# Kernel optimization log

Hardware: AMD Instinct MI355X
Metric: run time of the kernel (lower is better)

The kernel has to match this reference:

```python
import jax, jax.numpy as jnp
import numpy as np

H = 1024      # hidden_dim
F = 4 * H     # expert FFN dim
E = 16        # num_experts
K = 4         # num_experts_per_token


def setup_inputs() -> dict:
    key = jax.random.key(0)
    ks = jax.random.split(key, 10)
    s = 0.02
    return {
        "x": jax.random.normal(ks[0], (2, 1024, H), dtype=jnp.float32),
        # router: Linear(H,H) -> ReLU -> Linear(H,E)
        "Wr1": jax.random.normal(ks[1], (H, H), dtype=jnp.float32) * s,
        "br1": jnp.zeros((H,), dtype=jnp.float32),
        "Wr2": jax.random.normal(ks[2], (H, E), dtype=jnp.float32) * s,
        "br2": jnp.zeros((E,), dtype=jnp.float32),
        # stacked experts: Linear(H,4H) -> GELU -> Linear(4H,H)
        "W1": jax.random.normal(ks[3], (E, H, F), dtype=jnp.float32) * s,
        "b1": jnp.zeros((E, F), dtype=jnp.float32),
        "W2": jax.random.normal(ks[4], (E, F, H), dtype=jnp.float32) * s,
        "b2": jnp.zeros((E, H), dtype=jnp.float32),
    }


def reference(x, Wr1, br1, Wr2, br2, W1, b1, W2, b2):
    B, S, Hd = x.shape
    xf = x.reshape(-1, Hd)                       # [T, H]
    T = xf.shape[0]
    # router logits
    logits = jnp.maximum(xf @ Wr1 + br1, 0.0) @ Wr2 + br2   # [T, E]
    # top-k routing: softmax over the k selected logits
    topw, topi = jax.lax.top_k(logits, K)                    # [T, K]
    topw = jax.nn.softmax(topw, axis=-1)
    # dense combine weights c[t, e] = sum_k topw[t,k] * 1[topi[t,k]==e]
    c = jnp.zeros((T, E), dtype=xf.dtype)
    c = c.at[jnp.arange(T)[:, None], topi].add(topw)         # [T, E]
    # all-experts dense MLP (exact GELU, matching nn.GELU default)
    h = jax.nn.gelu(jnp.einsum('th,ehf->etf', xf, W1) + b1[:, None, :],
                    approximate=False)                       # [E, T, F]
    y = jnp.einsum('etf,efh->eth', h, W2) + b2[:, None, :]   # [E, T, H]
    out = jnp.einsum('eth,te->th', y, c)                     # [T, H]
    return out.reshape(B, S, Hd)
```

## Files before the change

### kernel.cpp

```cpp
#include <hip/hip_runtime.h>
#include <hip/hip_bf16.h>

#define T_TOK 2048
#define H_DIM 1024
#define F_DIM 4096
#define E_NUM 16
#define K_TOP 4

typedef float    floatx4 __attribute__((ext_vector_type(4)));
typedef _Float16 f16x8   __attribute__((ext_vector_type(8)));
typedef _Float16 f16x4   __attribute__((ext_vector_type(4)));

#define MiB (1024ull * 1024ull)
#define LOGIT_OFF ((size_t)0)
#define TOPI_OFF  (128ull * 1024)
#define TOPW_OFF  (192ull * 1024)
#define CNT_OFF   (256ull * 1024)
#define OFFS_OFF  (CNT_OFF + 256)
#define CUR_OFF   (OFFS_OFF + 256)
#define TOKS_OFF  (320ull * 1024)
#define WSL_OFF   (384ull * 1024)
#define STK_OFF   (448ull * 1024)
#define TILEE_OFF (512ull * 1024)
#define TILEM_OFF (TILEE_OFF + 512)
#define TILEC_OFF (TILEM_OFF + 512)
#define XH_OFF    (1ull * MiB)
#define HBUF_OFF  (8ull * MiB)
#define YBUF_OFF  (72ull * MiB)
#define W1T_OFF   (104ull * MiB)
#define W2T_OFF   (232ull * MiB)
#define WS_NEED_FAST (360ull * MiB)

__device__ __forceinline__ void gload16(const void* g, void* l) {
  __builtin_amdgcn_global_load_lds(
      (const __attribute__((address_space(1))) unsigned int*)g,
      (__attribute__((address_space(3))) unsigned int*)l, 16, 0, 0);
}

__device__ __forceinline__ float gelu_fast(float v) {
  float z = 0.7978845608028654f * (v + 0.044715f * v * v * v);
  float e = __expf(2.f * z);
  float t = 1.f - 2.f / (e + 1.f);
  return 0.5f * v * (1.f + t);
}

__global__ void zero_counts_kernel(int* counts) {
  if (threadIdx.x < E_NUM) counts[threadIdx.x] = 0;
}

__device__ __forceinline__ void cast_x_body(int blk, const float* __restrict__ x,
                                            _Float16* __restrict__ xh) {
  int i = blk * 256 + threadIdx.x;
  const floatx4* xin = reinterpret_cast<const floatx4*>(x) + (size_t)i * 2;
  floatx4 a = xin[0], b = xin[1];
  f16x8 o;
  o[0] = (_Float16)a[0]; o[1] = (_Float16)a[1]; o[2] = (_Float16)a[2]; o[3] = (_Float16)a[3];
  o[4] = (_Float16)b[0]; o[5] = (_Float16)b[1]; o[6] = (_Float16)b[2]; o[7] = (_Float16)b[3];
  *reinterpret_cast<f16x8*>(xh + (size_t)i * 8) = o;
}

__device__ __forceinline__ void tcast_body(const float* __restrict__ W,
                                           _Float16* __restrict__ Wt, int K, int N,
                                           int e, int k0, int n0, char* smem) {
  float (*Tt)[68] = (float(*)[68])smem;
  const float* We = W + (size_t)e * K * N;
  int t = threadIdx.x;
  int kk = t >> 4, nn = (t & 15) * 4;
#pragma unroll
  for (int j = 0; j < 4; j++) {
    int k = kk + 16 * j;
    floatx4 v = *reinterpret_cast<const floatx4*>(We + (size_t)(k0 + k) * N + n0 + nn);
    *reinterpret_cast<floatx4*>(&Tt[k][nn]) = v;
  }
  __syncthreads();
  int nr = t >> 2, kc = t & 3;
  f16x8 o0, o1;
#pragma unroll
  for (int j = 0; j < 8; j++) {
    o0[j] = (_Float16)Tt[kc * 16 + j][nr];
    o1[j] = (_Float16)Tt[kc * 16 + 8 + j][nr];
  }
  _Float16* dst = Wt + (size_t)e * N * K + (size_t)(n0 + nr) * K + k0 + kc * 16;
  *reinterpret_cast<f16x8*>(dst) = o0;
  *reinterpret_cast<f16x8*>(dst + 8) = o1;
}

__device__ __forceinline__ void router_gemm1_body(
    int m0, int n0, const float* __restrict__ x, const float* __restrict__ Wr1,
    const float* __restrict__ br1, float* __restrict__ hrf, char* smem) {
  _Float16 (*Ah)[40] = (_Float16(*)[40])(smem);
  _Float16 (*Al)[40] = (_Float16(*)[40])(smem + 5120);
  _Float16 (*Bh)[40] = (_Float16(*)[40])(smem + 10240);
  _Float16 (*Bl)[40] = (_Float16(*)[40])(smem + 15360);
  int tid = threadIdx.x;
  int arow = tid >> 2, achk = tid & 3;
  const float* Arow = x + (size_t)(m0 + arow) * H_DIM + achk * 8;
  int brow = tid >> 3, bq = tid & 7;

  floatx4 acc[2][2];
#pragma unroll
  for (int i = 0; i < 2; i++)
#pragma unroll
    for (int j = 0; j < 2; j++) acc[i][j] = (floatx4){0.f, 0.f, 0.f, 0.f};

  int wv = tid >> 6, lane = tid & 63;
  int wm = wv >> 1, wn = wv & 1;
  int lrow = lane & 15, lk = (lane >> 4) * 8;

  for (int k0 = 0; k0 < H_DIM; k0 += 32) {
    floatx4 a0 = *reinterpret_cast<const floatx4*>(Arow + k0);
    floatx4 a1 = *reinterpret_cast<const floatx4*>(Arow + k0 + 4);
    f16x8 hv, lv;
#pragma unroll
    for (int j = 0; j < 4; j++) {
      _Float16 hi = (_Float16)a0[j]; hv[j] = hi; lv[j] = (_Float16)(a0[j] - (float)hi);
      _Float16 hi2 = (_Float16)a1[j]; hv[4 + j] = hi2; lv[4 + j] = (_Float16)(a1[j] - (float)hi2);
    }
    *reinterpret_cast<f16x8*>(&Ah[arow][achk * 8]) = hv;
    *reinterpret_cast<f16x8*>(&Al[arow][achk * 8]) = lv;
    const float* wp = Wr1 + (size_t)(k0 + brow) * H_DIM + n0 + bq * 4;
    floatx4 w0 = *reinterpret_cast<const floatx4*>(wp);
    floatx4 w1 = *reinterpret_cast<const floatx4*>(wp + 32);
#pragma unroll
    for (int i = 0; i < 4; i++) {
      _Float16 h0 = (_Float16)w0[i];
      Bh[bq * 4 + i][brow] = h0; Bl[bq * 4 + i][brow] = (_Float16)(w0[i] - (float)h0);
      _Float16 h1 = (_Float16)w1[i];
      Bh[32 + bq * 4 + i][brow] = h1; Bl[32 + bq * 4 + i][brow] = (_Float16)(w1[i] - (float)h1);
    }
    __syncthreads();

    f16x8 ah0 = *reinterpret_cast<const f16x8*>(&Ah[32 * wm + lrow][lk]);
    f16x8 ah1 = *reinterpret_cast<const f16x8*>(&Ah[32 * wm + 16 + lrow][lk]);
    f16x8 al0 = *reinterpret_cast<const f16x8*>(&Al[32 * wm + lrow][lk]);
    f16x8 al1 = *reinterpret_cast<const f16x8*>(&Al[32 * wm + 16 + lrow][lk]);
    f16x8 bh0 = *reinterpret_cast<const f16x8*>(&Bh[32 * wn + lrow][lk]);
    f16x8 bh1 = *reinterpret_cast<const f16x8*>(&Bh[32 * wn + 16 + lrow][lk]);
    f16x8 bl0 = *reinterpret_cast<const f16x8*>(&Bl[32 * wn + lrow][lk]);
    f16x8 bl1 = *reinterpret_cast<const f16x8*>(&Bl[32 * wn + 16 + lrow][lk]);

    acc[0][0] = __builtin_amdgcn_mfma_f32_16x16x32_f16(ah0, bh0, acc[0][0], 0, 0, 0);
    acc[0][0] = __builtin_amdgcn_mfma_f32_16x16x32_f16(ah0, bl0, acc[0][0], 0, 0, 0);
    acc[0][0] = __builtin_amdgcn_mfma_f32_16x16x32_f16(al0, bh0, acc[0][0], 0, 0, 0);
    acc[0][1] = __builtin_amdgcn_mfma_f32_16x16x32_f16(ah0, bh1, acc[0][1], 0, 0, 0);
    acc[0][1] = __builtin_amdgcn_mfma_f32_16x16x32_f16(ah0, bl1, acc[0][1], 0, 0, 0);
    acc[0][1] = __builtin_amdgcn_mfma_f32_16x16x32_f16(al0, bh1, acc[0][1], 0, 0, 0);
    acc[1][0] = __builtin_amdgcn_mfma_f32_16x16x32_f16(ah1, bh0, acc[1][0], 0, 0, 0);
    acc[1][0] = __builtin_amdgcn_mfma_f32_16x16x32_f16(ah1, bl0, acc[1][0], 0, 0, 0);
    acc[1][0] = __builtin_amdgcn_mfma_f32_16x16x32_f16(al1, bh0, acc[1][0], 0, 0, 0);
    acc[1][1] = __builtin_amdgcn_mfma_f32_16x16x32_f16(ah1, bh1, acc[1][1], 0, 0, 0);
    acc[1][1] = __builtin_amdgcn_mfma_f32_16x16x32_f16(ah1, bl1, acc[1][1], 0, 0, 0);
    acc[1][1] = __builtin_amdgcn_mfma_f32_16x16x32_f16(al1, bh1, acc[1][1], 0, 0, 0);
    __syncthreads();
  }

#pragma unroll
  for (int am = 0; am < 2; am++) {
#pragma unroll
    for (int bn = 0; bn < 2; bn++) {
      int col = n0 + 32 * wn + 16 * bn + lrow;
      float bv = br1[col];
#pragma unroll
      for (int r = 0; r < 4; r++) {
        int rowt = 32 * wm + 16 * am + (lane >> 4) * 4 + r;
        float v = acc[am][bn][r] + bv;
        hrf[(size_t)(m0 + rowt) * H_DIM + col] = fmaxf(v, 0.f);
      }
    }
  }
}

#define FA_RG   512
#define FA_TC   16384
#define FA_CX   1024
__global__ __launch_bounds__(256) void fusedA_kernel(
    const float* __restrict__ x, const float* __restrict__ Wr1, const float* __restrict__ br1,
    float* __restrict__ hrf, const float* __restrict__ W1, _Float16* __restrict__ W1t,
    _Float16* __restrict__ xh) {
  __shared__ __align__(16) char smem[20480];
  int bid = blockIdx.x;
  if (bid < FA_RG) {
    router_gemm1_body((bid >> 4) * 64, (bid & 15) * 64, x, Wr1, br1, hrf, smem);
  } else if (bid < FA_RG + FA_TC) {
    int idx = bid - FA_RG;
    int nt = idx & 63, kt = (idx >> 6) & 15, e = idx >> 10;
    tcast_body(W1, W1t, H_DIM, F_DIM, e, kt * 64, nt * 64, smem);
  } else {
    cast_x_body(bid - FA_RG - FA_TC, x, xh);
  }
}

__global__ __launch_bounds__(256) void router_logits_kernel(
    const float* __restrict__ hrf, const float* __restrict__ Wr2,
    const float* __restrict__ br2, float* __restrict__ logits) {
  int t = blockIdx.x * 4 + (threadIdx.x >> 6);
  int lane = threadIdx.x & 63;
  float acc[E_NUM];
#pragma unroll
  for (int e = 0; e < E_NUM; e++) acc[e] = 0.f;
  const float* hr = hrf + (size_t)t * H_DIM;
#pragma unroll 4
  for (int i = 0; i < H_DIM / 64; i++) {
    int k = lane + 64 * i;
    float a = hr[k];
    const floatx4* w4 = reinterpret_cast<const floatx4*>(Wr2 + (size_t)k * E_NUM);
    floatx4 w0 = w4[0], w1 = w4[1], w2 = w4[2], w3 = w4[3];
#pragma unroll
    for (int j = 0; j < 4; j++) {
      acc[j]      += a * w0[j];
      acc[4 + j]  += a * w1[j];
      acc[8 + j]  += a * w2[j];
      acc[12 + j] += a * w3[j];
    }
  }
#pragma unroll
  for (int e = 0; e < E_NUM; e++) {
    float v = acc[e];
    for (int off = 32; off > 0; off >>= 1) v += __shfl_xor(v, off);
    if (lane == e) logits[(size_t)t * E_NUM + e] = v + br2[e];
  }
}

__global__ void route_kernel(const float* __restrict__ logits, int* __restrict__ topi,
                             float* __restrict__ topw, int* __restrict__ counts) {
  int t = blockIdx.x * 256 + threadIdx.x;
  if (t >= T_TOK) return;
  float lg[E_NUM];
#pragma unroll
  for (int e = 0; e < E_NUM; e++) lg[e] = logits[(size_t)t * E_NUM + e];
  unsigned int used = 0;
  float vals[K_TOP]; int idx[K_TOP];
#pragma unroll
  for (int k = 0; k < K_TOP; k++) {
    float best = -1e30f; int bi = 0;
#pragma unroll
    for (int e = 0; e < E_NUM; e++) {
      if (!((used >> e) & 1u) && lg[e] > best) { best = lg[e]; bi = e; }
    }
    used |= (1u << bi);
    vals[k] = best; idx[k] = bi;
  }
  float m = vals[0];
  float s = 0.f;
  float w[K_TOP];
#pragma unroll
  for (int k = 0; k < K_TOP; k++) { w[k] = expf(vals[k] - m); s += w[k]; }
  float inv = 1.f / s;
#pragma unroll
  for (int k = 0; k < K_TOP; k++) {
    topi[t * K_TOP + k] = idx[k];
    topw[t * K_TOP + k] = w[k] * inv;
    atomicAdd(&counts[idx[k]], 1);
  }
}

__global__ void scan_kernel(const int* __restrict__ counts, int* __restrict__ offsets,
                            int* __restrict__ cursor, int* __restrict__ tileE,
                            int* __restrict__ tileM, int* __restrict__ tileC) {
  if (threadIdx.x == 0) {
    int acc = 0;
    offsets[0] = 0;
    for (int e = 0; e < E_NUM; e++) { acc += counts[e]; offsets[e + 1] = acc; }
    int idx = 0;
    for (int e = 0; e < E_NUM; e++) {
      int c = counts[e];
      for (int m0 = 0; m0 < c; m0 += 128) { tileE[idx] = e; tileM[idx] = m0; idx++; }
    }
    tileC[0] = idx;
  }
  if (threadIdx.x < E_NUM) cursor[threadIdx.x] = 0;
}

__global__ void scatter_kernel(const int* __restrict__ topi, const float* __restrict__ topw,
                               const int* __restrict__ offsets, int* __restrict__ cursor,
                               int* __restrict__ tok_of_slot, float* __restrict__ w_of_slot,
                               int* __restrict__ slot_of_tk) {
  int t = blockIdx.x * 256 + threadIdx.x;
  if (t >= T_TOK) return;
#pragma unroll
  for (int k = 0; k < K_TOP; k++) {
    int e = topi[t * K_TOP + k];
    int pos = atomicAdd(&cursor[e], 1);
    int slot = offsets[e] + pos;
    tok_of_slot[slot] = t;
    w_of_slot[slot] = topw[t * K_TOP + k];
    slot_of_tk[t * K_TOP + k] = slot;
  }
}

__global__ void combine_kernel(const float* __restrict__ ybuf, const int* __restrict__ slot_of_tk,
                               float* __restrict__ out) {
  int i = blockIdx.x * 256 + threadIdx.x;
  size_t p = (size_t)i * 4;
  int t = (int)(p >> 10);
  int h = (int)(p & 1023);
  float s0 = 0.f, s1 = 0.f, s2 = 0.f, s3 = 0.f;
#pragma unroll
  for (int k = 0; k < K_TOP; k++) {
    int slot = slot_of_tk[t * K_TOP + k];
    const floatx4 v = *reinterpret_cast<const floatx4*>(ybuf + (size_t)slot * H_DIM + h);
    s0 += v[0]; s1 += v[1]; s2 += v[2]; s3 += v[3];
  }
  floatx4 o = {s0, s1, s2, s3};
  *reinterpret_cast<floatx4*>(out + p) = o;
}

template <int ACT, bool GATHER, bool SCALE, bool OUTF16>
__device__ __forceinline__ void moe_gemm_body(
    int ti, int n0, const _Float16* __restrict__ A, const _Float16* __restrict__ Bt,
    const float* __restrict__ bias, void* __restrict__ Out,
    const int* __restrict__ offsets, const int* __restrict__ toklist,
    const float* __restrict__ wslot, const int* __restrict__ tileE,
    const int* __restrict__ tileM, const int* __restrict__ tileC,
    int N, int K, char* smem) {
  if (ti >= tileC[0]) return;
  int e = tileE[ti], m0 = tileM[ti];
  int base = offsets[e], cnt = offsets[e + 1] - base;

  _Float16 (*As)[128][32] = (_Float16(*)[128][32])(smem);
  _Float16 (*Bs)[128][32] = (_Float16(*)[128][32])(smem + 16384);

  int tid = threadIdx.x;
  int w = tid >> 6, lane = tid & 63;
  int wm = w >> 1, wn = w & 1;
  int lrow = lane & 15, lkc = (lane >> 4) * 8;

  int ar0 = w * 32 + (lane >> 2);
  int ar1 = ar0 + 16;
  int ach = (lane & 3) * 8;
  int mr0 = m0 + ar0; if (mr0 >= cnt) mr0 = cnt - 1;
  int mr1 = m0 + ar1; if (mr1 >= cnt) mr1 = cnt - 1;
  const _Float16* gA0 = A + (long)(GATHER ? toklist[base + mr0] : (base + mr0)) * K + ach;
  const _Float16* gA1 = A + (long)(GATHER ? toklist[base + mr1] : (base + mr1)) * K + ach;
  const _Float16* bge = Bt + (size_t)e * N * K;
  const _Float16* gB0 = bge + (long)(n0 + ar0) * K + ach;
  const _Float16* gB1 = bge + (long)(n0 + ar1) * K + ach;

#define STAGE2(buf, kk) do { \
    gload16(gA0 + (kk), &As[buf][w * 32][0]); \
    gload16(gA1 + (kk), &As[buf][w * 32 + 16][0]); \
    gload16(gB0 + (kk), &Bs[buf][w * 32][0]); \
    gload16(gB1 + (kk), &Bs[buf][w * 32 + 16][0]); \
  } while (0)

  floatx4 acc[4][4];
#pragma unroll
  for (int i = 0; i < 4; i++)
#pragma unroll
    for (int j = 0; j < 4; j++) acc[i][j] = (floatx4){0.f, 0.f, 0.f, 0.f};

  STAGE2(0, 0);
  __syncthreads();

  int nk = K >> 5;
  for (int it = 0; it < nk; ++it) {
    int cur = it & 1;
    if (it + 1 < nk) STAGE2(cur ^ 1, (it + 1) << 5);

    f16x8 a[4], b[4];
#pragma unroll
    for (int i = 0; i < 4; i++) {
      a[i] = *reinterpret_cast<const f16x8*>(&As[cur][wm * 64 + i * 16 + lrow][lkc]);
      b[i] = *reinterpret_cast<const f16x8*>(&Bs[cur][wn * 64 + i * 16 + lrow][lkc]);
    }
#pragma unroll
    for (int i = 0; i < 4; i++)
#pragma unroll
      for (int j = 0; j < 4; j++)
        acc[i][j] = __builtin_amdgcn_mfma_f32_16x16x32_f16(a[i], b[j], acc[i][j], 0, 0, 0);

    __syncthreads();
  }
#undef STAGE2

  const float* be = bias + (size_t)e * N;
#pragma unroll
  for (int fm = 0; fm < 4; fm++) {
#pragma unroll
    for (int fn = 0; fn < 4; fn++) {
      int col = n0 + wn * 64 + fn * 16 + lrow;
      float bv = be[col];
#pragma unroll
      for (int r = 0; r < 4; r++) {
        int rowt = wm * 64 + fm * 16 + (lane >> 4) * 4 + r;
        int mg = m0 + rowt;
        if (mg < cnt) {
          float v = acc[fm][fn][r] + bv;
          if (ACT == 2) v = gelu_fast(v);
          long orow = base + mg;
          if (SCALE) v *= wslot[orow];
          if (OUTF16)
            ((_Float16*)Out)[orow * (long)N + col] = (_Float16)v;
          else
            ((float*)Out)[orow * (long)N + col] = v;
        }
      }
    }
  }
}

#define FB_G1 (32 * 80)
#define FB_TC 16384
__global__ __launch_bounds__(256) void fusedB_kernel(
    const _Float16* __restrict__ xh, const _Float16* __restrict__ W1t,
    const float* __restrict__ b1, _Float16* __restrict__ hbuf,
    const int* __restrict__ offsets, const int* __restrict__ toklist,
    const int* __restrict__ tileE, const int* __restrict__ tileM, const int* __restrict__ tileC,
    const float* __restrict__ W2, _Float16* __restrict__ W2t) {
  __shared__ __align__(16) char smem[32768];
  int bid = blockIdx.x;
  if (bid < FB_G1) {
    moe_gemm_body<2, true, false, true>(bid >> 5, (bid & 31) * 128, xh, W1t, b1, (void*)hbuf,
                                        offsets, toklist, nullptr, tileE, tileM, tileC,
                                        F_DIM, H_DIM, smem);
  } else {
    int idx = bid - FB_G1;
    int nt = idx & 15, kt = (idx >> 4) & 63, e = idx >> 10;
    tcast_body(W2, W2t, F_DIM, H_DIM, e, kt * 64, nt * 64, smem);
  }
}

__global__ __launch_bounds__(256) void moe_gemm2_kernel(
    const _Float16* __restrict__ hbuf, const _Float16* __restrict__ W2t,
    const float* __restrict__ b2, float* __restrict__ ybuf,
    const int* __restrict__ offsets, const float* __restrict__ wslot,
    const int* __restrict__ tileE, const int* __restrict__ tileM, const int* __restrict__ tileC) {
  __shared__ __align__(16) char smem[32768];
  moe_gemm_body<0, false, true, false>(blockIdx.y, blockIdx.x * 128, hbuf, W2t, b2, (void*)ybuf,
                                       offsets, nullptr, wslot, tileE, tileM, tileC,
                                       H_DIM, F_DIM, smem);
}

template <int ACT, bool GATHER, bool OFFS, bool SCALE, bool OUTF16>
__global__ __launch_bounds__(256) void moe_gemm(
    const _Float16* __restrict__ A, const float* __restrict__ W,
    const float* __restrict__ bias, void* __restrict__ Out,
    const int* __restrict__ offsets, const int* __restrict__ toklist,
    const float* __restrict__ wslot, int M, int N, int K) {
  int e = blockIdx.z;
  int base = 0, cnt = M;
  if (OFFS) { base = offsets[e]; cnt = offsets[e + 1] - base; }
  int m0 = blockIdx.y * 64;
  if (m0 >= cnt) return;
  int n0 = blockIdx.x * 64;
  const float* We = W + (size_t)e * K * N;
  const float* be = bias + (size_t)e * N;

  __shared__ _Float16 As[64][40];
  __shared__ _Float16 Bs[64][40];

  int tid = threadIdx.x;
  int arow = tid >> 2, achk = tid & 3;
  int am_idx = m0 + arow; if (am_idx > cnt - 1) am_idx = cnt - 1;
  long arowg = GATHER ? (long)toklist[base + am_idx] : (long)(base + am_idx);
  const _Float16* Arow = A + arowg * (long)K + achk * 8;

  int brow = tid >> 3, bq = tid & 7;

  floatx4 acc[2][2];
#pragma unroll
  for (int i = 0; i < 2; i++)
#pragma unroll
    for (int j = 0; j < 2; j++) acc[i][j] = (floatx4){0.f, 0.f, 0.f, 0.f};

  int wv = tid >> 6, lane = tid & 63;
  int wm = wv >> 1, wn = wv & 1;
  int lrow = lane & 15, lk = (lane >> 4) * 8;

  for (int k0 = 0; k0 < K; k0 += 32) {
    *reinterpret_cast<f16x8*>(&As[arow][achk * 8]) = *reinterpret_cast<const f16x8*>(Arow + k0);
    const float* wp = We + (size_t)(k0 + brow) * N + n0 + bq * 4;
    floatx4 w0 = *reinterpret_cast<const floatx4*>(wp);
    floatx4 w1 = *reinterpret_cast<const floatx4*>(wp + 32);
#pragma unroll
    for (int i = 0; i < 4; i++) {
      Bs[bq * 4 + i][brow]      = (_Float16)w0[i];
      Bs[32 + bq * 4 + i][brow] = (_Float16)w1[i];
    }
    __syncthreads();

    f16x8 a0 = *reinterpret_cast<const f16x8*>(&As[32 * wm + lrow][lk]);
    f16x8 a1 = *reinterpret_cast<const f16x8*>(&As[32 * wm + 16 + lrow][lk]);
    f16x8 b0 = *reinterpret_cast<const f16x8*>(&Bs[32 * wn + lrow][lk]);
    f16x8 b1 = *reinterpret_cast<const f16x8*>(&Bs[32 * wn + 16 + lrow][lk]);
    acc[0][0] = __builtin_amdgcn_mfma_f32_16x16x32_f16(a0, b0, acc[0][0], 0, 0, 0);
    acc[0][1] = __builtin_amdgcn_mfma_f32_16x16x32_f16(a0, b1, acc[0][1], 0, 0, 0);
    acc[1][0] = __builtin_amdgcn_mfma_f32_16x16x32_f16(a1, b0, acc[1][0], 0, 0, 0);
    acc[1][1] = __builtin_amdgcn_mfma_f32_16x16x32_f16(a1, b1, acc[1][1], 0, 0, 0);
    __syncthreads();
  }

#pragma unroll
  for (int am = 0; am < 2; am++) {
#pragma unroll
    for (int bn = 0; bn < 2; bn++) {
      int col = n0 + 32 * wn + 16 * bn + lrow;
      float bv = be[col];
#pragma unroll
      for (int r = 0; r < 4; r++) {
        int rowt = 32 * wm + 16 * am + (lane >> 4) * 4 + r;
        int mg = m0 + rowt;
        if (mg < cnt) {
          float v = acc[am][bn][r] + bv;
          if (ACT == 2) v = gelu_fast(v);
          long orow = base + mg;
          if (SCALE) v *= wslot[orow];
          if (OUTF16)
            ((_Float16*)Out)[orow * (long)N + col] = (_Float16)v;
          else
            ((float*)Out)[orow * (long)N + col] = v;
        }
      }
    }
  }
}

__global__ void cast_x_kernel(const float* __restrict__ x, _Float16* __restrict__ xh) {
  cast_x_body(blockIdx.x, x, xh);
}

__global__ __launch_bounds__(256) void router_gemm1_kernel(
    const float* __restrict__ x, const float* __restrict__ Wr1,
    const float* __restrict__ br1, float* __restrict__ hrf) {
  __shared__ __align__(16) char smem[20480];
  router_gemm1_body(blockIdx.y * 64, blockIdx.x * 64, x, Wr1, br1, hrf, smem);
}

extern "C" void kernel_launch(void* const* d_in, const int* in_sizes, int n_in,
                              void* d_out, int out_size, void* d_ws, size_t ws_size,
                              hipStream_t stream) {
  const float* x   = (const float*)d_in[0];
  const float* Wr1 = (const float*)d_in[1];
  const float* br1 = (const float*)d_in[2];
  const float* Wr2 = (const float*)d_in[3];
  const float* br2 = (const float*)d_in[4];
  const float* W1  = (const float*)d_in[5];
  const float* b1  = (const float*)d_in[6];
  const float* W2  = (const float*)d_in[7];
  const float* b2  = (const float*)d_in[8];
  float* out = (float*)d_out;

  char* ws = (char*)d_ws;
  float* logits = (float*)(ws + LOGIT_OFF);
  int*   topi   = (int*)(ws + TOPI_OFF);
  float* topw   = (float*)(ws + TOPW_OFF);
  int*   counts = (int*)(ws + CNT_OFF);
  int*   offs   = (int*)(ws + OFFS_OFF);
  int*   cursor = (int*)(ws + CUR_OFF);
  int*   toks   = (int*)(ws + TOKS_OFF);
  float* wsl    = (float*)(ws + WSL_OFF);
  int*   stk    = (int*)(ws + STK_OFF);
  int*   tileE  = (int*)(ws + TILEE_OFF);
  int*   tileM  = (int*)(ws + TILEM_OFF);
  int*   tileC  = (int*)(ws + TILEC_OFF);
  _Float16* xh   = (_Float16*)(ws + XH_OFF);
  float*    hrf  = (float*)(ws + HBUF_OFF);
  _Float16* hbuf = (_Float16*)(ws + HBUF_OFF);
  float*    ybuf = (float*)(ws + YBUF_OFF);
  _Float16* W1t  = (_Float16*)(ws + W1T_OFF);
  _Float16* W2t  = (_Float16*)(ws + W2T_OFF);

  bool fast = ws_size >= WS_NEED_FAST;

  zero_counts_kernel<<<1, 64, 0, stream>>>(counts);

  if (fast) {
    fusedA_kernel<<<FA_RG + FA_TC + FA_CX, 256, 0, stream>>>(x, Wr1, br1, hrf, W1, W1t, xh);
  } else {
    cast_x_kernel<<<(T_TOK * H_DIM / 8) / 256, 256, 0, stream>>>(x, xh);
    router_gemm1_kernel<<<dim3(H_DIM / 64, T_TOK / 64), 256, 0, stream>>>(x, Wr1, br1, hrf);
  }

  router_logits_kernel<<<T_TOK / 4, 256, 0, stream>>>(hrf, Wr2, br2, logits);
  route_kernel<<<T_TOK / 256, 256, 0, stream>>>(logits, topi, topw, counts);
  scan_kernel<<<1, 64, 0, stream>>>(counts, offs, cursor, tileE, tileM, tileC);
  scatter_kernel<<<T_TOK / 256, 256, 0, stream>>>(topi, topw, offs, cursor, toks, wsl, stk);

  if (fast) {
    fusedB_kernel<<<FB_G1 + FB_TC, 256, 0, stream>>>(xh, W1t, b1, hbuf, offs, toks,
                                                     tileE, tileM, tileC, W2, W2t);
    moe_gemm2_kernel<<<dim3(H_DIM / 128, 80), 256, 0, stream>>>(hbuf, W2t, b2, ybuf, offs, wsl,
                                                                tileE, tileM, tileC);
  } else {
    moe_gemm<2, true, true, false, true><<<dim3(F_DIM / 64, T_TOK / 64, E_NUM), 256, 0, stream>>>(
        xh, W1, b1, (void*)hbuf, offs, toks, nullptr, T_TOK, F_DIM, H_DIM);
    moe_gemm<0, false, true, true, false><<<dim3(H_DIM / 64, T_TOK / 64, E_NUM), 256, 0, stream>>>(
        hbuf, W2, b2, (void*)ybuf, offs, nullptr, wsl, T_TOK, H_DIM, F_DIM);
  }

  combine_kernel<<<(T_TOK * H_DIM / 4) / 256, 256, 0, stream>>>(ybuf, stk, out);
}
```

Baseline: 496.1 us.

## Fuse routing into one kernel, triple-buffer MoE GEMMs with LDS swizzle, fp16 ybuf

Merges the zero-count, route, scan and scatter kernels into a single 1024-thread block that uses shared-memory counters, removing four launches. The grouped expert GEMM moves from a double-buffered loop with a full barrier each step to a three-stage global-to-LDS pipeline with vmcnt waits, an XOR swizzle to cut LDS bank conflicts, and raised MFMA priority. The expert output buffer becomes fp16, halving traffic for the second GEMM's stores and the combine reads. Risks include extra precision loss in y, more LDS per block lowering occupancy, and the hand-written vmcnt/barrier synchronisation.

```diff
diff --git a/kernel.cpp b/kernel.cpp
--- a/kernel.cpp
+++ b/kernel.cpp
@@ -13,11 +13,7 @@
 
 #define MiB (1024ull * 1024ull)
 #define LOGIT_OFF ((size_t)0)
-#define TOPI_OFF  (128ull * 1024)
-#define TOPW_OFF  (192ull * 1024)
-#define CNT_OFF   (256ull * 1024)
-#define OFFS_OFF  (CNT_OFF + 256)
-#define CUR_OFF   (OFFS_OFF + 256)
+#define OFFS_OFF  (256ull * 1024)
 #define TOKS_OFF  (320ull * 1024)
 #define WSL_OFF   (384ull * 1024)
 #define STK_OFF   (448ull * 1024)
@@ -42,10 +38,6 @@
   float e = __expf(2.f * z);
   float t = 1.f - 2.f / (e + 1.f);
   return 0.5f * v * (1.f + t);
-}
-
-__global__ void zero_counts_kernel(int* counts) {
-  if (threadIdx.x < E_NUM) counts[threadIdx.x] = 0;
 }
 
 __device__ __forceinline__ void cast_x_body(int blk, const float* __restrict__ x,
@@ -221,113 +213,114 @@
   }
 }
 
-__global__ void route_kernel(const float* __restrict__ logits, int* __restrict__ topi,
-                             float* __restrict__ topw, int* __restrict__ counts) {
-  int t = blockIdx.x * 256 + threadIdx.x;
-  if (t >= T_TOK) return;
-  float lg[E_NUM];
-#pragma unroll
-  for (int e = 0; e < E_NUM; e++) lg[e] = logits[(size_t)t * E_NUM + e];
-  unsigned int used = 0;
-  float vals[K_TOP]; int idx[K_TOP];
-#pragma unroll
-  for (int k = 0; k < K_TOP; k++) {
-    float best = -1e30f; int bi = 0;
-#pragma unroll
-    for (int e = 0; e < E_NUM; e++) {
-      if (!((used >> e) & 1u) && lg[e] > best) { best = lg[e]; bi = e; }
-    }
-    used |= (1u << bi);
-    vals[k] = best; idx[k] = bi;
-  }
-  float m = vals[0];
-  float s = 0.f;
-  float w[K_TOP];
-#pragma unroll
-  for (int k = 0; k < K_TOP; k++) { w[k] = expf(vals[k] - m); s += w[k]; }
-  float inv = 1.f / s;
-#pragma unroll
-  for (int k = 0; k < K_TOP; k++) {
-    topi[t * K_TOP + k] = idx[k];
-    topw[t * K_TOP + k] = w[k] * inv;
-    atomicAdd(&counts[idx[k]], 1);
-  }
-}
-
-__global__ void scan_kernel(const int* __restrict__ counts, int* __restrict__ offsets,
-                            int* __restrict__ cursor, int* __restrict__ tileE,
-                            int* __restrict__ tileM, int* __restrict__ tileC) {
-  if (threadIdx.x == 0) {
+__global__ __launch_bounds__(1024) void routing_kernel(
+    const float* __restrict__ logits, int* __restrict__ offs,
+    int* __restrict__ toks, float* __restrict__ wsl, int* __restrict__ stk,
+    int* __restrict__ tileE, int* __restrict__ tileM, int* __restrict__ tileC) {
+  __shared__ int cnt[E_NUM], cur[E_NUM], loff[E_NUM + 1];
+  int tid = threadIdx.x;
+  if (tid < E_NUM) { cnt[tid] = 0; cur[tid] = 0; }
+  __syncthreads();
+  int ti[2][K_TOP]; float tw[2][K_TOP];
+#pragma unroll
+  for (int u = 0; u < 2; u++) {
+    int t = u * 1024 + tid;
+    float lg[E_NUM];
+#pragma unroll
+    for (int e = 0; e < E_NUM; e++) lg[e] = logits[(size_t)t * E_NUM + e];
+    unsigned int used = 0;
+    float vals[K_TOP];
+#pragma unroll
+    for (int k = 0; k < K_TOP; k++) {
+      float best = -1e30f; int bi = 0;
+#pragma unroll
+      for (int e = 0; e < E_NUM; e++) {
+        if (!((used >> e) & 1u) && lg[e] > best) { best = lg[e]; bi = e; }
+      }
+      used |= (1u << bi);
+      vals[k] = best; ti[u][k] = bi;
+    }
+    float m = vals[0], s = 0.f;
+#pragma unroll
+    for (int k = 0; k < K_TOP; k++) { tw[u][k] = expf(vals[k] - m); s += tw[u][k]; }
+    float inv = 1.f / s;
+#pragma unroll
+    for (int k = 0; k < K_TOP; k++) {
+      tw[u][k] *= inv;
+      atomicAdd(&cnt[ti[u][k]], 1);
+    }
+  }
+  __syncthreads();
+  if (tid == 0) {
     int acc = 0;
-    offsets[0] = 0;
-    for (int e = 0; e < E_NUM; e++) { acc += counts[e]; offsets[e + 1] = acc; }
+    loff[0] = 0; offs[0] = 0;
+    for (int e = 0; e < E_NUM; e++) { acc += cnt[e]; loff[e + 1] = acc; offs[e + 1] = acc; }
     int idx = 0;
     for (int e = 0; e < E_NUM; e++) {
-      int c = counts[e];
-      for (int m0 = 0; m0 < c; m0 += 128) { tileE[idx] = e; tileM[idx] = m0; idx++; }
+      for (int m0 = 0; m0 < cnt[e]; m0 += 128) { tileE[idx] = e; tileM[idx] = m0; idx++; }
     }
     tileC[0] = idx;
   }
-  if (threadIdx.x < E_NUM) cursor[threadIdx.x] = 0;
-}
-
-__global__ void scatter_kernel(const int* __restrict__ topi, const float* __restrict__ topw,
-                               const int* __restrict__ offsets, int* __restrict__ cursor,
-                               int* __restrict__ tok_of_slot, float* __restrict__ w_of_slot,
-                               int* __restrict__ slot_of_tk) {
-  int t = blockIdx.x * 256 + threadIdx.x;
-  if (t >= T_TOK) return;
-#pragma unroll
-  for (int k = 0; k < K_TOP; k++) {
-    int e = topi[t * K_TOP + k];
-    int pos = atomicAdd(&cursor[e], 1);
-    int slot = offsets[e] + pos;
-    tok_of_slot[slot] = t;
-    w_of_slot[slot] = topw[t * K_TOP + k];
-    slot_of_tk[t * K_TOP + k] = slot;
-  }
-}
-
-__global__ void combine_kernel(const float* __restrict__ ybuf, const int* __restrict__ slot_of_tk,
+  __syncthreads();
+#pragma unroll
+  for (int u = 0; u < 2; u++) {
+    int t = u * 1024 + tid;
+#pragma unroll
+    for (int k = 0; k < K_TOP; k++) {
+      int e = ti[u][k];
+      int pos = atomicAdd(&cur[e], 1);
+      int slot = loff[e] + pos;
+      toks[slot] = t;
+      wsl[slot] = tw[u][k];
+      stk[t * K_TOP + k] = slot;
+    }
+  }
+}
+
+__global__ void combine_kernel(const _Float16* __restrict__ ybuf, const int* __restrict__ stk,
                                float* __restrict__ out) {
   int i = blockIdx.x * 256 + threadIdx.x;
-  size_t p = (size_t)i * 4;
+  size_t p = (size_t)i * 8;
   int t = (int)(p >> 10);
   int h = (int)(p & 1023);
-  float s0 = 0.f, s1 = 0.f, s2 = 0.f, s3 = 0.f;
+  float s[8] = {0.f, 0.f, 0.f, 0.f, 0.f, 0.f, 0.f, 0.f};
 #pragma unroll
   for (int k = 0; k < K_TOP; k++) {
-    int slot = slot_of_tk[t * K_TOP + k];
-    const floatx4 v = *reinterpret_cast<const floatx4*>(ybuf + (size_t)slot * H_DIM + h);
-    s0 += v[0]; s1 += v[1]; s2 += v[2]; s3 += v[3];
-  }
-  floatx4 o = {s0, s1, s2, s3};
-  *reinterpret_cast<floatx4*>(out + p) = o;
-}
-
-template <int ACT, bool GATHER, bool SCALE, bool OUTF16>
+    int slot = stk[t * K_TOP + k];
+    f16x8 v = *reinterpret_cast<const f16x8*>(ybuf + (size_t)slot * H_DIM + h);
+#pragma unroll
+    for (int j = 0; j < 8; j++) s[j] += (float)v[j];
+  }
+  floatx4 o0 = {s[0], s[1], s[2], s[3]};
+  floatx4 o1 = {s[4], s[5], s[6], s[7]};
+  *reinterpret_cast<floatx4*>(out + p) = o0;
+  *reinterpret_cast<floatx4*>(out + p + 4) = o1;
+}
+
+template <int KK, int ACT, bool GATHER, bool SCALE>
 __device__ __forceinline__ void moe_gemm_body(
     int ti, int n0, const _Float16* __restrict__ A, const _Float16* __restrict__ Bt,
-    const float* __restrict__ bias, void* __restrict__ Out,
+    const float* __restrict__ bias, _Float16* __restrict__ Out,
     const int* __restrict__ offsets, const int* __restrict__ toklist,
     const float* __restrict__ wslot, const int* __restrict__ tileE,
     const int* __restrict__ tileM, const int* __restrict__ tileC,
-    int N, int K, char* smem) {
+    int N, char* smem) {
   if (ti >= tileC[0]) return;
+  const int K = KK;
   int e = tileE[ti], m0 = tileM[ti];
   int base = offsets[e], cnt = offsets[e + 1] - base;
 
-  _Float16 (*As)[128][32] = (_Float16(*)[128][32])(smem);
-  _Float16 (*Bs)[128][32] = (_Float16(*)[128][32])(smem + 16384);
+  _Float16 (*As)[128][32] = reinterpret_cast<_Float16(*)[128][32]>(smem);
+  _Float16 (*Bs)[128][32] = reinterpret_cast<_Float16(*)[128][32]>(smem + 24576);
 
   int tid = threadIdx.x;
   int w = tid >> 6, lane = tid & 63;
   int wm = w >> 1, wn = w & 1;
-  int lrow = lane & 15, lkc = (lane >> 4) * 8;
+  int lrow = lane & 15;
 
   int ar0 = w * 32 + (lane >> 2);
   int ar1 = ar0 + 16;
-  int ach = (lane & 3) * 8;
+  int ach = (((lane & 3) ^ ((lane >> 3) & 3))) * 8;
   int mr0 = m0 + ar0; if (mr0 >= cnt) mr0 = cnt - 1;
   int mr1 = m0 + ar1; if (mr1 >= cnt) mr1 = cnt - 1;
   const _Float16* gA0 = A + (long)(GATHER ? toklist[base + mr0] : (base + mr0)) * K + ach;
@@ -336,42 +329,54 @@
   const _Float16* gB0 = bge + (long)(n0 + ar0) * K + ach;
   const _Float16* gB1 = bge + (long)(n0 + ar1) * K + ach;
 
-#define STAGE2(buf, kk) do { \
+  int phys8 = ((lane >> 4) ^ ((lrow >> 1) & 3)) * 8;
+
+#define STAGE3(buf, kk) do { \
     gload16(gA0 + (kk), &As[buf][w * 32][0]); \
     gload16(gA1 + (kk), &As[buf][w * 32 + 16][0]); \
     gload16(gB0 + (kk), &Bs[buf][w * 32][0]); \
     gload16(gB1 + (kk), &Bs[buf][w * 32 + 16][0]); \
   } while (0)
 
+#define COMPUTE3(buf) do { \
+    f16x8 a[4], b[4]; \
+    _Pragma("unroll") \
+    for (int i = 0; i < 4; i++) { \
+      a[i] = *reinterpret_cast<const f16x8*>(&As[buf][wm * 64 + i * 16 + lrow][phys8]); \
+      b[i] = *reinterpret_cast<const f16x8*>(&Bs[buf][wn * 64 + i * 16 + lrow][phys8]); \
+    } \
+    __builtin_amdgcn_s_setprio(1); \
+    _Pragma("unroll") \
+    for (int i = 0; i < 4; i++) \
+      _Pragma("unroll") \
+      for (int j = 0; j < 4; j++) \
+        acc[i][j] = __builtin_amdgcn_mfma_f32_16x16x32_f16(a[i], b[j], acc[i][j], 0, 0, 0); \
+    __builtin_amdgcn_s_setprio(0); \
+  } while (0)
+
   floatx4 acc[4][4];
 #pragma unroll
   for (int i = 0; i < 4; i++)
 #pragma unroll
     for (int j = 0; j < 4; j++) acc[i][j] = (floatx4){0.f, 0.f, 0.f, 0.f};
 
-  STAGE2(0, 0);
-  __syncthreads();
-
-  int nk = K >> 5;
-  for (int it = 0; it < nk; ++it) {
-    int cur = it & 1;
-    if (it + 1 < nk) STAGE2(cur ^ 1, (it + 1) << 5);
-
-    f16x8 a[4], b[4];
-#pragma unroll
-    for (int i = 0; i < 4; i++) {
-      a[i] = *reinterpret_cast<const f16x8*>(&As[cur][wm * 64 + i * 16 + lrow][lkc]);
-      b[i] = *reinterpret_cast<const f16x8*>(&Bs[cur][wn * 64 + i * 16 + lrow][lkc]);
-    }
-#pragma unroll
-    for (int i = 0; i < 4; i++)
-#pragma unroll
-      for (int j = 0; j < 4; j++)
-        acc[i][j] = __builtin_amdgcn_mfma_f32_16x16x32_f16(a[i], b[j], acc[i][j], 0, 0, 0);
-
-    __syncthreads();
-  }
-#undef STAGE2
+  constexpr int nk = KK / 32;
+  STAGE3(0, 0);
+  STAGE3(1, 32);
+
+#pragma unroll 3
+  for (int it = 0; it < nk - 1; ++it) {
+    asm volatile("s_waitcnt vmcnt(4)" ::: "memory");
+    __builtin_amdgcn_s_barrier();
+    if (it + 2 < nk) STAGE3((it + 2) % 3, (it + 2) * 32);
+    COMPUTE3(it % 3);
+  }
+  asm volatile("s_waitcnt vmcnt(0)" ::: "memory");
+  __builtin_amdgcn_s_barrier();
+  COMPUTE3((nk - 1) % 3);
+
+#undef STAGE3
+#undef COMPUTE3
 
   const float* be = bias + (size_t)e * N;
 #pragma unroll
@@ -389,10 +394,7 @@
           if (ACT == 2) v = gelu_fast(v);
           long orow = base + mg;
           if (SCALE) v *= wslot[orow];
-          if (OUTF16)
-            ((_Float16*)Out)[orow * (long)N + col] = (_Float16)v;
-          else
-            ((float*)Out)[orow * (long)N + col] = v;
+          Out[orow * (long)N + col] = (_Float16)v;
         }
       }
     }
@@ -407,12 +409,12 @@
     const int* __restrict__ offsets, const int* __restrict__ toklist,
     const int* __restrict__ tileE, const int* __restrict__ tileM, const int* __restrict__ tileC,
     const float* __restrict__ W2, _Float16* __restrict__ W2t) {
-  __shared__ __align__(16) char smem[32768];
+  __shared__ __align__(16) char smem[49152];
   int bid = blockIdx.x;
   if (bid < FB_G1) {
-    moe_gemm_body<2, true, false, true>(bid >> 5, (bid & 31) * 128, xh, W1t, b1, (void*)hbuf,
-                                        offsets, toklist, nullptr, tileE, tileM, tileC,
-                                        F_DIM, H_DIM, smem);
+    moe_gemm_body<H_DIM, 2, true, false>(bid >> 5, (bid & 31) * 128, xh, W1t, b1, hbuf,
+                                         offsets, toklist, nullptr, tileE, tileM, tileC,
+                                         F_DIM, smem);
   } else {
     int idx = bid - FB_G1;
     int nt = idx & 15, kt = (idx >> 4) & 63, e = idx >> 10;
@@ -422,19 +424,19 @@
 
 __global__ __launch_bounds__(256) void moe_gemm2_kernel(
     const _Float16* __restrict__ hbuf, const _Float16* __restrict__ W2t,
-    const float* __restrict__ b2, float* __restrict__ ybuf,
+    const float* __restrict__ b2, _Float16* __restrict__ ybuf,
     const int* __restrict__ offsets, const float* __restrict__ wslot,
     const int* __restrict__ tileE, const int* __restrict__ tileM, const int* __restrict__ tileC) {
-  __shared__ __align__(16) char smem[32768];
-  moe_gemm_body<0, false, true, false>(blockIdx.y, blockIdx.x * 128, hbuf, W2t, b2, (void*)ybuf,
+  __shared__ __align__(16) char smem[49152];
+  moe_gemm_body<F_DIM, 0, false, true>(blockIdx.y, blockIdx.x * 128, hbuf, W2t, b2, ybuf,
                                        offsets, nullptr, wslot, tileE, tileM, tileC,
-                                       H_DIM, F_DIM, smem);
-}
-
-template <int ACT, bool GATHER, bool OFFS, bool SCALE, bool OUTF16>
+                                       H_DIM, smem);
+}
+
+template <int ACT, bool GATHER, bool OFFS, bool SCALE>
 __global__ __launch_bounds__(256) void moe_gemm(
     const _Float16* __restrict__ A, const float* __restrict__ W,
-    const float* __restrict__ bias, void* __restrict__ Out,
+    const float* __restrict__ bias, _Float16* __restrict__ Out,
     const int* __restrict__ offsets, const int* __restrict__ toklist,
     const float* __restrict__ wslot, int M, int N, int K) {
   int e = blockIdx.z;
@@ -505,10 +507,7 @@
           if (ACT == 2) v = gelu_fast(v);
           long orow = base + mg;
           if (SCALE) v *= wslot[orow];
-          if (OUTF16)
-            ((_Float16*)Out)[orow * (long)N + col] = (_Float16)v;
-          else
-            ((float*)Out)[orow * (long)N + col] = v;
+          Out[orow * (long)N + col] = (_Float16)v;
         }
       }
     }
@@ -542,11 +541,7 @@
 
   char* ws = (char*)d_ws;
   float* logits = (float*)(ws + LOGIT_OFF);
-  int*   topi   = (int*)(ws + TOPI_OFF);
-  float* topw   = (float*)(ws + TOPW_OFF);
-  int*   counts = (int*)(ws + CNT_OFF);
   int*   offs   = (int*)(ws + OFFS_OFF);
-  int*   cursor = (int*)(ws + CUR_OFF);
   int*   toks   = (int*)(ws + TOKS_OFF);
   float* wsl    = (float*)(ws + WSL_OFF);
   int*   stk    = (int*)(ws + STK_OFF);
@@ -556,13 +551,11 @@
   _Float16* xh   = (_Float16*)(ws + XH_OFF);
   float*    hrf  = (float*)(ws + HBUF_OFF);
   _Float16* hbuf = (_Float16*)(ws + HBUF_OFF);
-  float*    ybuf = (float*)(ws + YBUF_OFF);
+  _Float16* ybuf = (_Float16*)(ws + YBUF_OFF);
   _Float16* W1t  = (_Float16*)(ws + W1T_OFF);
   _Float16* W2t  = (_Float16*)(ws + W2T_OFF);
 
   bool fast = ws_size >= WS_NEED_FAST;
-
-  zero_counts_kernel<<<1, 64, 0, stream>>>(counts);
 
   if (fast) {
     fusedA_kernel<<<FA_RG + FA_TC + FA_CX, 256, 0, stream>>>(x, Wr1, br1, hrf, W1, W1t, xh);
@@ -572,9 +565,7 @@
   }
 
   router_logits_kernel<<<T_TOK / 4, 256, 0, stream>>>(hrf, Wr2, br2, logits);
-  route_kernel<<<T_TOK / 256, 256, 0, stream>>>(logits, topi, topw, counts);
-  scan_kernel<<<1, 64, 0, stream>>>(counts, offs, cursor, tileE, tileM, tileC);
-  scatter_kernel<<<T_TOK / 256, 256, 0, stream>>>(topi, topw, offs, cursor, toks, wsl, stk);
+  routing_kernel<<<1, 1024, 0, stream>>>(logits, offs, toks, wsl, stk, tileE, tileM, tileC);
 
   if (fast) {
     fusedB_kernel<<<FB_G1 + FB_TC, 256, 0, stream>>>(xh, W1t, b1, hbuf, offs, toks,
@@ -582,11 +573,11 @@
     moe_gemm2_kernel<<<dim3(H_DIM / 128, 80), 256, 0, stream>>>(hbuf, W2t, b2, ybuf, offs, wsl,
                                                                 tileE, tileM, tileC);
   } else {
-    moe_gemm<2, true, true, false, true><<<dim3(F_DIM / 64, T_TOK / 64, E_NUM), 256, 0, stream>>>(
-        xh, W1, b1, (void*)hbuf, offs, toks, nullptr, T_TOK, F_DIM, H_DIM);
-    moe_gemm<0, false, true, true, false><<<dim3(H_DIM / 64, T_TOK / 64, E_NUM), 256, 0, stream>>>(
-        hbuf, W2, b2, (void*)ybuf, offs, nullptr, wsl, T_TOK, H_DIM, F_DIM);
-  }
-
-  combine_kernel<<<(T_TOK * H_DIM / 4) / 256, 256, 0, stream>>>(ybuf, stk, out);
-}
+    moe_gemm<2, true, true, false><<<dim3(F_DIM / 64, T_TOK / 64, E_NUM), 256, 0, stream>>>(
+        xh, W1, b1, hbuf, offs, toks, nullptr, T_TOK, F_DIM, H_DIM);
+    moe_gemm<0, false, true, true><<<dim3(H_DIM / 64, T_TOK / 64, E_NUM), 256, 0, stream>>>(
+        hbuf, W2, b2, ybuf, offs, nullptr, wsl, T_TOK, H_DIM, F_DIM);
+  }
+
+  combine_kernel<<<(T_TOK * H_DIM / 8) / 256, 256, 0, stream>>>(ybuf, stk, out);
+}
```

Result: faster. 454.1 us (-8.5%).
